# Kernel optimization log

Measured on AMD Instinct MI355X. Metric: run time of the kernel, lower is better.

## Reference

```python
import jax, jax.numpy as jnp
import numpy as np

Cin, E, L, M, H, Cout = 256, 16, 64, 64, 64, 256
B, N = 16, 2048
D = M + L * E  # hypernetwork input dim = 1088


def setup_inputs() -> dict:
    key = jax.random.key(0)
    ks = jax.random.split(key, 8)
    def lin(k, fan_in, shape):
        return jax.random.normal(k, shape, jnp.float32) / np.float32(np.sqrt(fan_in))
    return {
        "x0": jax.random.randint(ks[0], (B, N), 0, Cin),
        "emb": jax.random.normal(ks[1], (Cin, E), jnp.float32) * 0.02,
        "W_enc_w": lin(ks[2], D, (D, H)), "W_enc_b": jnp.zeros((H,), jnp.float32),
        "W_dec_w": lin(ks[3], H, (H, M * M)), "W_dec_b": jnp.zeros((M * M,), jnp.float32),
        "b_enc_w": lin(ks[4], D, (D, H)), "b_enc_b": jnp.zeros((H,), jnp.float32),
        "b_dec_w": lin(ks[5], H, (H, M)), "b_dec_b": jnp.zeros((M,), jnp.float32),
        "dec_w": lin(ks[6], M, (M, Cout)), "dec_b": jnp.zeros((Cout,), jnp.float32),
    }


def reference(x0, emb, W_enc_w, W_enc_b, W_dec_w, W_dec_b,
              b_enc_w, b_enc_b, b_dec_w, b_dec_b, dec_w, dec_b):
    Bq, Nq = x0.shape
    inv_ln2 = jnp.float32(1.0 / np.log(2.0))
    # left-pad with token id 0 (torch pad on int indices pads zeros -> embedding row 0)
    xp = jnp.concatenate([jnp.zeros((Bq, L), x0.dtype), x0], axis=-1)  # [B, N+L]
    e = emb[xp]  # [B, N+L, E]
    # window for step t = tokens t-L..t-1 of x0 = xp[:, t:t+L]
    idxs = jnp.arange(Nq)[:, None] + jnp.arange(L)[None, :]  # [N, L]
    win = e[:, idxs].reshape(Bq, Nq, L * E).transpose(1, 0, 2)  # [N, B, L*E]
    ys = x0.T  # [N, B]

    def mlp(x, ew, eb, dw, db):
        return jax.nn.sigmoid(x @ ew + eb) @ dw + db

    def step(m, xy):
        w, y = xy  # w: [B, L*E], y: [B]
        inp = jnp.concatenate([m, w], axis=-1)  # [B, M + L*E]
        Wm = mlp(inp, W_enc_w, W_enc_b, W_dec_w, W_dec_b).reshape(Bq, M, M)
        bm = mlp(inp, b_enc_w, b_enc_b, b_dec_w, b_dec_b)  # [B, M]
        m = jax.nn.sigmoid(jnp.einsum('bij,bj->bi', Wm, m) + bm)
        logits = m @ dec_w + dec_b  # [B, Cout]
        lse = jax.nn.log_softmax(logits)
        loss = -jnp.take_along_axis(lse, y[:, None], axis=1)[:, 0] * inv_ln2
        return m, loss

    m0 = jnp.zeros((Bq, M), jnp.float32)
    _, losses = jax.lax.scan(step, m0, (win, ys))  # losses: [N, B]
    return losses.reshape(-1)  # matches torch.cat(losses): time-major [N*B]
```

## Files before the change

### kernel.cpp

```cpp
#include <hip/hip_runtime.h>
#include <hip/hip_bf16.h>
#include <hip/hip_fp16.h>


typedef unsigned int uint_t;
typedef unsigned short us_t;
typedef unsigned long long u64_t;
typedef _Float16 h2_t __attribute__((ext_vector_type(2)));

#define POISON64 0xAAAAAAAAAAAAAAAAULL

__device__ __forceinline__ us_t f2bf(float f) {
    uint_t u = __float_as_uint(f);
    uint_t r = u + 0x7fffu + ((u >> 16) & 1u);
    return (us_t)(r >> 16);
}
__device__ __forceinline__ float bf2f(us_t s) {
    return __uint_as_float(((uint_t)s) << 16);
}
__device__ __forceinline__ float bflo(uint_t u) { return __uint_as_float(u << 16); }
__device__ __forceinline__ float bfhi(uint_t u) { return __uint_as_float(u & 0xffff0000u); }

__device__ __forceinline__ us_t f2h(float f) {
    __half h = __float2half(f);
    return *reinterpret_cast<us_t*>(&h);
}
__device__ __forceinline__ float h2f(us_t s) {
    __half h = *reinterpret_cast<__half*>(&s);
    return __half2float(h);
}
__device__ __forceinline__ h2_t u2h2(uint_t u) {
    union { uint_t u; h2_t h; } x; x.u = u; return x.h;
}

#if __has_builtin(__builtin_amdgcn_fdot2)
__device__ __forceinline__ float dot2f(uint_t a, uint_t b, float c) {
    return __builtin_amdgcn_fdot2(u2h2(a), u2h2(b), c, false);
}
#else
__device__ __forceinline__ float dot2f(uint_t a, uint_t b, float c) {
    h2_t x = u2h2(a), y = u2h2(b);
    return c + (float)x.x * (float)y.x + (float)x.y * (float)y.y;
}
#endif

#define DOT4(q, base, acc)                                              \
    acc = dot2f(q.x, mreg2u[(base) + 0], acc);                          \
    acc = dot2f(q.y, mreg2u[(base) + 1], acc);                          \
    acc = dot2f(q.z, mreg2u[(base) + 2], acc);                          \
    acc = dot2f(q.w, mreg2u[(base) + 3], acc);

__global__ void cvt_kernel(const float* __restrict__ Wdecw,
                           const float* __restrict__ decw,
                           const float* __restrict__ Wencw,
                           const float* __restrict__ bencw,
                           us_t* __restrict__ WdG, us_t* __restrict__ decwY,
                           us_t* __restrict__ EWmG) {
    int o = blockIdx.x * 256 + threadIdx.x;
    if (o < 262144) {
        int s = o >> 16;
        int idx = o & 65535;
        int k = idx & 7;
        int oo = (idx >> 3) & 1023;
        int jp = idx >> 13;
        int h = oo >> 4, il = oo & 15;
        int i = s * 16 + il;
        int j = jp * 8 + k;
        WdG[o] = f2h(Wdecw[h * 4096 + i * 64 + j]);
    } else if (o < 278528) {
        int oo = o - 262144;
        int k = oo & 3, lane = (oo >> 2) & 63, mm = oo >> 8;
        decwY[oo] = f2bf(decw[mm * 256 + k * 64 + lane]);
    } else if (o < 286720) {
        int oo = o - 278528;
        int kk = oo & 7, h2 = (oo >> 3) & 127, jp = oo >> 10;
        int j = jp * 8 + kk;
        float v = (h2 < 64) ? Wencw[j * 64 + h2] : bencw[j * 64 + (h2 - 64)];
        EWmG[oo] = f2h(v);
    }
}

__global__ void build_T(const float* __restrict__ emb, const float* __restrict__ Wencw,
                        const float* __restrict__ bencw, float* __restrict__ T) {
    int l = blockIdx.x >> 8, v = blockIdx.x & 255, h2 = threadIdx.x;
    float acc = 0.f;
#pragma unroll
    for (int e = 0; e < 16; ++e) {
        int d = 64 + l * 16 + e;
        float w = (h2 < 64) ? Wencw[d * 64 + h2] : bencw[d * 64 + (h2 - 64)];
        acc += emb[v * 16 + e] * w;
    }
    T[blockIdx.x * 128 + h2] = acc;
}

__global__ void build_P(const float* __restrict__ T, const int* __restrict__ x0,
                        const float* __restrict__ Wencb, const float* __restrict__ bencb,
                        float* __restrict__ P) {
    int t = blockIdx.x >> 4, b = blockIdx.x & 15, h2 = threadIdx.x;
    float acc = (h2 < 64) ? Wencb[h2] : bencb[h2 - 64];
    for (int l = 0; l < 64; ++l) {
        int p = t + l;
        int v = (p < 64) ? 0 : x0[b * 2048 + (p - 64)];
        acc += T[(l * 256 + v) * 128 + h2];
    }
    P[blockIdx.x * 128 + h2] = acc;
}

__global__ __launch_bounds__(512, 2) void recur(
    const float* __restrict__ bdecw, const float* __restrict__ bdecb,
    const float* __restrict__ Wdecb, const us_t* __restrict__ WdG,
    const us_t* __restrict__ EWmG, const float* __restrict__ P,
    u64_t* __restrict__ mhb) {
    const int b = blockIdx.x & 15, s = blockIdx.x >> 4;
    const int tid = threadIdx.x;

    extern __shared__ char smem[];
    us_t*   EWm2   = (us_t*)(smem + 131072);
    us_t*   wdbt_s = (us_t*)(smem + 147456);
    us_t*   bdec_s = (us_t*)(smem + 149632);
    float*  hw_s   = (float*)(smem + 151808);
    float*  hb_s   = (float*)(smem + 152064);
    float*  m_s    = (float*)(smem + 152320);
    float*  V_s    = (float*)(smem + 152576);
    float*  rp_s   = (float*)(smem + 156928);
    float*  bias_s = (float*)(smem + 157440);
    uint_t* m2_s   = (uint_t*)(smem + 157504);

    uint4 wreg[16];
    {
        const uint4* g4 = (const uint4*)WdG + s * 8192;
#pragma unroll
        for (int jp = 0; jp < 8; ++jp) {
            wreg[jp]     = g4[jp * 1024 + tid];
            wreg[8 + jp] = g4[jp * 1024 + tid + 512];
        }
    }
    {
        const uint4* g4 = (const uint4*)EWmG;
        uint4* l4 = (uint4*)EWm2;
        for (int k = tid; k < 1024; k += 512) l4[k] = g4[k];
    }
    for (int k = tid; k < 1024; k += 512) {
        int j = k >> 4, il = k & 15;
        wdbt_s[j * 17 + il] = f2bf(Wdecb[(s * 16 + il) * 64 + j]);
        bdec_s[j * 17 + il] = f2bf(bdecw[j * 64 + s * 16 + il]);
    }
    if (tid < 16) bias_s[tid] = bdecb[s * 16 + tid];
    if (tid < 64) m_s[tid] = 0.f;
    if (tid < 32) m2_s[tid] = 0u;
    __syncthreads();

    uint_t mreg2u[32];
#pragma unroll
    for (int j = 0; j < 32; ++j) mreg2u[j] = 0u;

    float preg = 0.f;
    if (tid < 128) preg = P[b * 128 + tid];

    const uint4* EW4 = (const uint4*)EWm2;
    const int hA = tid >> 4, ilA = tid & 15;

    for (int t = 0; t < 2048; ++t) {
        float pnext = 0.f;
        int tp = (t < 2047) ? (t + 1) : 2047;
        if (tid < 128) pnext = P[(tp * 16 + b) * 128 + tid];

        float a0 = 0.f, a1 = 0.f;
#pragma unroll
        for (int jp = 0; jp < 8; ++jp) {
            uint4 q0 = wreg[jp];
            uint4 q1 = wreg[8 + jp];
            DOT4(q0, jp * 4, a0);
            DOT4(q1, jp * 4, a1);
        }
        V_s[hA * 17 + ilA] = a0;
        V_s[(hA + 32) * 17 + ilA] = a1;

        if (tid < 128) {
            float acc = preg;
#pragma unroll
            for (int jp = 0; jp < 8; ++jp) {
                uint4 e = EW4[jp * 128 + tid];
                DOT4(e, jp * 4, acc);
            }
            float sg = 1.f / (1.f + __expf(-acc));
            if (tid < 64) hw_s[tid] = sg; else hb_s[tid - 64] = sg;
        }
        preg = pnext;
        __syncthreads();

        if (tid < 128) {
            int il = tid & 15, q = (tid >> 4) & 3;
            if (tid < 64) {
                float r = 0.f;
#pragma unroll
                for (int hh = 0; hh < 16; ++hh) {
                    int h = q * 16 + hh;
                    r += hw_s[h] * V_s[h * 17 + il];
                }
                rp_s[q * 16 + il] = r;
            } else {
                float r = 0.f;
#pragma unroll
                for (int kk = 0; kk < 16; ++kk) {
                    int jh = q * 16 + kk;
                    r += m_s[jh] * bf2f(wdbt_s[jh * 17 + il]);
                    r += hb_s[jh] * bf2f(bdec_s[jh * 17 + il]);
                }
                rp_s[64 + q * 16 + il] = r;
            }
        }
        __syncthreads();

        if (tid < 64) {
            u64_t* row = mhb + (u64_t)(t * 16 + b) * 16;
            float nmf = 0.f;
            if (tid < 16) {
                float r = bias_s[tid];
#pragma unroll
                for (int p = 0; p < 8; ++p) r += rp_s[p * 16 + tid];
                nmf = 1.f / (1.f + __expf(-r));
            }
            us_t nh = f2h(nmf);
            if (tid < 16) m_s[s * 16 + tid] = h2f(nh);
            uint_t nhu = (uint_t)nh;
            uint_t w0 = (uint_t)__shfl((int)nhu, (tid & 3) * 4 + 0, 64);
            uint_t w1 = (uint_t)__shfl((int)nhu, (tid & 3) * 4 + 1, 64);
            uint_t w2 = (uint_t)__shfl((int)nhu, (tid & 3) * 4 + 2, 64);
            uint_t w3 = (uint_t)__shfl((int)nhu, (tid & 3) * 4 + 3, 64);
            if (tid < 4) {
                u64_t pay = (u64_t)w0 | ((u64_t)w1 << 16)
                          | ((u64_t)w2 << 32) | ((u64_t)w3 << 48);
                __hip_atomic_store(row + s * 4 + tid, pay,
                                   __ATOMIC_RELAXED, __HIP_MEMORY_SCOPE_AGENT);
            }
            const bool self = (tid >> 2) == s;
            u64_t vk = 0;
            for (;;) {
                if (tid < 16 && !self)
                    vk = __hip_atomic_load(row + tid, __ATOMIC_RELAXED,
                                           __HIP_MEMORY_SCOPE_AGENT);
                bool ok = (tid >= 16) || self || (vk != POISON64);
                if (__ballot(ok) == ~0ull) break;
                __builtin_amdgcn_s_sleep(1);
            }
            if (tid < 16 && !self) {
                float4 mv;
                mv.x = h2f((us_t)(vk & 0xFFFFu));
                mv.y = h2f((us_t)((vk >> 16) & 0xFFFFu));
                mv.z = h2f((us_t)((vk >> 32) & 0xFFFFu));
                mv.w = h2f((us_t)(vk >> 48));
                ((float4*)m_s)[tid] = mv;
            }
            __builtin_amdgcn_s_waitcnt(0xC07F);
            if (tid < 32) {
                uint_t pk = (uint_t)f2h(m_s[2 * tid])
                          | ((uint_t)f2h(m_s[2 * tid + 1]) << 16);
                m2_s[tid] = pk;
            }
        }
        __syncthreads();

        {
            const uint4* mg = (const uint4*)m2_s;
#pragma unroll
            for (int p = 0; p < 8; ++p) {
                uint4 v = mg[p];
                mreg2u[p * 4 + 0] = v.x;
                mreg2u[p * 4 + 1] = v.y;
                mreg2u[p * 4 + 2] = v.z;
                mreg2u[p * 4 + 3] = v.w;
            }
        }
    }
}

__global__ __launch_bounds__(256) void loss_kernel(
    const us_t* __restrict__ mhb, const us_t* __restrict__ decwY,
    const float* __restrict__ decb, const int* __restrict__ x0,
    float* __restrict__ out) {
    __shared__ __align__(16) us_t dw[16384];
    const int tid = threadIdx.x;
    {
        const uint4* g4 = (const uint4*)decwY;
        uint4* l4 = (uint4*)dw;
        for (int k = tid; k < 2048; k += 256) l4[k] = g4[k];
    }
    __syncthreads();
    const int lane = tid & 63, wv = tid >> 6;
    const uint2* dwu2 = (const uint2*)dw;
    float b0 = decb[lane], b1 = decb[lane + 64];
    float b2 = decb[lane + 128], b3 = decb[lane + 192];
    for (int r = 0; r < 8; ++r) {
        int row = blockIdx.x * 32 + wv * 8 + r;
        float mL = h2f(mhb[row * 64 + lane]);
        float l0 = b0, l1 = b1, l2 = b2, l3 = b3;
#pragma unroll
        for (int mm = 0; mm < 64; ++mm) {
            float mv = __shfl(mL, mm, 64);
            uint2 q = dwu2[mm * 64 + lane];
            l0 += mv * bflo(q.x);
            l1 += mv * bfhi(q.x);
            l2 += mv * bflo(q.y);
            l3 += mv * bfhi(q.y);
        }
        float mx = fmaxf(fmaxf(l0, l1), fmaxf(l2, l3));
#pragma unroll
        for (int o = 32; o > 0; o >>= 1) mx = fmaxf(mx, __shfl_xor(mx, o, 64));
        float se = __expf(l0 - mx) + __expf(l1 - mx) + __expf(l2 - mx) + __expf(l3 - mx);
#pragma unroll
        for (int o = 32; o > 0; o >>= 1) se += __shfl_xor(se, o, 64);
        float lse = mx + __logf(se);
        int t = row >> 4, bb = row & 15;
        int y = x0[bb * 2048 + t];
        int hi = y >> 6;
        float cand = hi == 0 ? l0 : (hi == 1 ? l1 : (hi == 2 ? l2 : l3));
        float ly = __shfl(cand, y & 63, 64);
        if (lane == 0) out[row] = (lse - ly) * 1.4426950408889634f;
    }
}

extern "C" void kernel_launch(void* const* d_in, const int* in_sizes, int n_in,
                              void* d_out, int out_size, void* d_ws, size_t ws_size,
                              hipStream_t stream) {
    const int*   x0    = (const int*)d_in[0];
    const float* emb   = (const float*)d_in[1];
    const float* Wencw = (const float*)d_in[2];
    const float* Wencb = (const float*)d_in[3];
    const float* Wdecw = (const float*)d_in[4];
    const float* Wdecb = (const float*)d_in[5];
    const float* bencw = (const float*)d_in[6];
    const float* bencb = (const float*)d_in[7];
    const float* bdecw = (const float*)d_in[8];
    const float* bdecb = (const float*)d_in[9];
    const float* decw  = (const float*)d_in[10];
    const float* decb  = (const float*)d_in[11];
    float* out = (float*)d_out;

    char* ws = (char*)d_ws;
    us_t*  WdG   = (us_t*)(ws);
    us_t*  decwY = (us_t*)(ws + 524288);
    us_t*  EWmG  = (us_t*)(ws + 557056);
    float* T     = (float*)(ws + 573440);
    u64_t* mhb   = (u64_t*)T;
    float* P     = (float*)(ws + 8962048);

    static const int kRecurLds = 157632;
    (void)hipFuncSetAttribute((const void*)recur,
                              hipFuncAttributeMaxDynamicSharedMemorySize,
                              kRecurLds);

    cvt_kernel<<<1120, 256, 0, stream>>>(Wdecw, decw, Wencw, bencw,
                                         WdG, decwY, EWmG);
    build_T<<<16384, 128, 0, stream>>>(emb, Wencw, bencw, T);
    build_P<<<32768, 128, 0, stream>>>(T, x0, Wencb, bencb, P);
    (void)hipMemsetAsync(mhb, 0xAA, 4194304, stream);
    recur<<<64, 512, kRecurLds, stream>>>(bdecw, bdecb, Wdecb, WdG, EWmG,
                                          P, mhb);
    loss_kernel<<<1024, 256, 0, stream>>>((const us_t*)mhb, decwY, decb, x0, out);
}
```

Before: 3.964 ms.

## Split hypernetwork weight slice by hidden unit and exchange partial sums across blocks

```diff
diff --git a/kernel.cpp b/kernel.cpp
--- a/kernel.cpp
+++ b/kernel.cpp
@@ -8,15 +8,10 @@
 typedef unsigned long long u64_t;
 typedef _Float16 h2_t __attribute__((ext_vector_type(2)));
 
-#define POISON64 0xAAAAAAAAAAAAAAAAULL
-
 __device__ __forceinline__ us_t f2bf(float f) {
     uint_t u = __float_as_uint(f);
     uint_t r = u + 0x7fffu + ((u >> 16) & 1u);
     return (us_t)(r >> 16);
-}
-__device__ __forceinline__ float bf2f(us_t s) {
-    return __uint_as_float(((uint_t)s) << 16);
 }
 __device__ __forceinline__ float bflo(uint_t u) { return __uint_as_float(u << 16); }
 __device__ __forceinline__ float bfhi(uint_t u) { return __uint_as_float(u & 0xffff0000u); }
@@ -63,8 +58,8 @@
         int k = idx & 7;
         int oo = (idx >> 3) & 1023;
         int jp = idx >> 13;
-        int h = oo >> 4, il = oo & 15;
-        int i = s * 16 + il;
+        int h = s * 16 + (oo >> 6);
+        int i = oo & 63;
         int j = jp * 8 + k;
         WdG[o] = f2h(Wdecw[h * 4096 + i * 64 + j]);
     } else if (o < 278528) {
@@ -110,21 +105,22 @@
     const float* __restrict__ bdecw, const float* __restrict__ bdecb,
     const float* __restrict__ Wdecb, const us_t* __restrict__ WdG,
     const us_t* __restrict__ EWmG, const float* __restrict__ P,
-    u64_t* __restrict__ mhb) {
+    uint_t* __restrict__ mh32, u64_t* __restrict__ pxb) {
     const int b = blockIdx.x & 15, s = blockIdx.x >> 4;
     const int tid = threadIdx.x;
 
     extern __shared__ char smem[];
-    us_t*   EWm2   = (us_t*)(smem + 131072);
-    us_t*   wdbt_s = (us_t*)(smem + 147456);
-    us_t*   bdec_s = (us_t*)(smem + 149632);
-    float*  hw_s   = (float*)(smem + 151808);
-    float*  hb_s   = (float*)(smem + 152064);
-    float*  m_s    = (float*)(smem + 152320);
-    float*  V_s    = (float*)(smem + 152576);
-    float*  rp_s   = (float*)(smem + 156928);
-    float*  bias_s = (float*)(smem + 157440);
-    uint_t* m2_s   = (uint_t*)(smem + 157504);
+    us_t*   EWm2   = (us_t*)(smem);
+    uint_t* wdbt2  = (uint_t*)(smem + 16384);
+    uint_t* bdec2  = (uint_t*)(smem + 24576);
+    float*  V_s    = (float*)(smem + 32768);
+    float*  rp4_s  = (float*)(smem + 36928);
+    float*  wdbm2_s= (float*)(smem + 37952);
+    float*  hbb2_s = (float*)(smem + 38464);
+    float*  hw_s   = (float*)(smem + 38976);
+    uint_t* hb2_s  = (uint_t*)(smem + 39232);
+    uint_t* m2_s   = (uint_t*)(smem + 39360);
+    float*  bias_s = (float*)(smem + 39488);
 
     uint4 wreg[16];
     {
@@ -140,13 +136,14 @@
         uint4* l4 = (uint4*)EWm2;
         for (int k = tid; k < 1024; k += 512) l4[k] = g4[k];
     }
-    for (int k = tid; k < 1024; k += 512) {
-        int j = k >> 4, il = k & 15;
-        wdbt_s[j * 17 + il] = f2bf(Wdecb[(s * 16 + il) * 64 + j]);
-        bdec_s[j * 17 + il] = f2bf(bdecw[j * 64 + s * 16 + il]);
-    }
-    if (tid < 16) bias_s[tid] = bdecb[s * 16 + tid];
-    if (tid < 64) m_s[tid] = 0.f;
+    for (int k = tid; k < 2048; k += 512) {
+        int jj = k >> 6, i = k & 63;
+        wdbt2[k] = (uint_t)f2h(Wdecb[i * 64 + 2 * jj])
+                 | ((uint_t)f2h(Wdecb[i * 64 + 2 * jj + 1]) << 16);
+        bdec2[k] = (uint_t)f2h(bdecw[(2 * jj) * 64 + i])
+                 | ((uint_t)f2h(bdecw[(2 * jj + 1) * 64 + i]) << 16);
+    }
+    if (tid < 64) bias_s[tid] = bdecb[tid];
     if (tid < 32) m2_s[tid] = 0u;
     __syncthreads();
 
@@ -158,7 +155,8 @@
     if (tid < 128) preg = P[b * 128 + tid];
 
     const uint4* EW4 = (const uint4*)EWm2;
-    const int hA = tid >> 4, ilA = tid & 15;
+    const int hl = tid >> 6, iA = tid & 63;
+    const int w = tid >> 6;
 
     for (int t = 0; t < 2048; ++t) {
         float pnext = 0.f;
@@ -173,8 +171,8 @@
             DOT4(q0, jp * 4, a0);
             DOT4(q1, jp * 4, a1);
         }
-        V_s[hA * 17 + ilA] = a0;
-        V_s[(hA + 32) * 17 + ilA] = a1;
+        V_s[hl * 65 + iA] = a0;
+        V_s[(hl + 8) * 65 + iA] = a1;
 
         if (tid < 128) {
             float acc = preg;
@@ -184,79 +182,86 @@
                 DOT4(e, jp * 4, acc);
             }
             float sg = 1.f / (1.f + __expf(-acc));
-            if (tid < 64) hw_s[tid] = sg; else hb_s[tid - 64] = sg;
+            if (tid < 64) {
+                hw_s[tid] = sg;
+            } else {
+                int l = tid - 64;
+                float vlo = __shfl(sg, (l & 31) * 2, 64);
+                float vhi = __shfl(sg, (l & 31) * 2 + 1, 64);
+                if (l < 32)
+                    hb2_s[l] = (uint_t)f2h(vlo) | ((uint_t)f2h(vhi) << 16);
+            }
         }
         preg = pnext;
         __syncthreads();
 
-        if (tid < 128) {
-            int il = tid & 15, q = (tid >> 4) & 3;
-            if (tid < 64) {
-                float r = 0.f;
-#pragma unroll
-                for (int hh = 0; hh < 16; ++hh) {
-                    int h = q * 16 + hh;
-                    r += hw_s[h] * V_s[h * 17 + il];
+        u64_t* slotb = pxb + (u64_t)(((t & 1) * 16 + b) * 4) * 64;
+        const uint_t tg = (uint_t)(t + 1);
+
+        if (tid < 64) {
+            float r0 = 0.f, r1 = 0.f;
+#pragma unroll
+            for (int hh = 0; hh < 8; ++hh) {
+                r0 += hw_s[s * 16 + 2 * hh]     * V_s[(2 * hh) * 65 + tid];
+                r1 += hw_s[s * 16 + 2 * hh + 1] * V_s[(2 * hh + 1) * 65 + tid];
+            }
+            float rs = r0 + r1;
+            rp4_s[s * 64 + tid] = rs;
+            u64_t pay = ((u64_t)tg << 32) | (u64_t)__float_as_uint(rs);
+            __hip_atomic_store(slotb + s * 64 + tid, pay,
+                               __ATOMIC_RELAXED, __HIP_MEMORY_SCOPE_AGENT);
+        }
+
+        if (w < 3) {
+            int p = w + (w >= s ? 1 : 0);
+            int lane = tid & 63;
+            const u64_t* src = slotb + p * 64 + lane;
+            u64_t v;
+            for (;;) {
+                v = __hip_atomic_load(src, __ATOMIC_RELAXED,
+                                      __HIP_MEMORY_SCOPE_AGENT);
+                if (__ballot((uint_t)(v >> 32) == tg) == ~0ull) break;
+                __builtin_amdgcn_s_sleep(1);
+            }
+            rp4_s[p * 64 + lane] = __uint_as_float((uint_t)v);
+        } else if (w < 5) {
+            int i = tid & 63;
+            float wm = 0.f, hbv = 0.f;
+            if (w == 3) {
+#pragma unroll
+                for (int jj = 0; jj < 16; ++jj) {
+                    wm  = dot2f(wdbt2[jj * 64 + i], mreg2u[jj], wm);
+                    hbv = dot2f(bdec2[jj * 64 + i], hb2_s[jj], hbv);
                 }
-                rp_s[q * 16 + il] = r;
+                wdbm2_s[i] = wm;
+                hbb2_s[i] = hbv;
             } else {
-                float r = 0.f;
-#pragma unroll
-                for (int kk = 0; kk < 16; ++kk) {
-                    int jh = q * 16 + kk;
-                    r += m_s[jh] * bf2f(wdbt_s[jh * 17 + il]);
-                    r += hb_s[jh] * bf2f(bdec_s[jh * 17 + il]);
+#pragma unroll
+                for (int jj = 0; jj < 16; ++jj) {
+                    wm  = dot2f(wdbt2[(16 + jj) * 64 + i], mreg2u[16 + jj], wm);
+                    hbv = dot2f(bdec2[(16 + jj) * 64 + i], hb2_s[16 + jj], hbv);
                 }
-                rp_s[64 + q * 16 + il] = r;
+                wdbm2_s[64 + i] = wm;
+                hbb2_s[64 + i] = hbv;
             }
         }
         __syncthreads();
 
         if (tid < 64) {
-            u64_t* row = mhb + (u64_t)(t * 16 + b) * 16;
-            float nmf = 0.f;
-            if (tid < 16) {
-                float r = bias_s[tid];
-#pragma unroll
-                for (int p = 0; p < 8; ++p) r += rp_s[p * 16 + tid];
-                nmf = 1.f / (1.f + __expf(-r));
-            }
-            us_t nh = f2h(nmf);
-            if (tid < 16) m_s[s * 16 + tid] = h2f(nh);
+            float r = ((rp4_s[tid] + rp4_s[64 + tid])
+                     + (rp4_s[128 + tid] + rp4_s[192 + tid]))
+                    + (wdbm2_s[tid] + wdbm2_s[64 + tid])
+                    + (hbb2_s[tid] + hbb2_s[64 + tid])
+                    + bias_s[tid];
+            float nm = 1.f / (1.f + __expf(-r));
+            us_t nh = f2h(nm);
             uint_t nhu = (uint_t)nh;
-            uint_t w0 = (uint_t)__shfl((int)nhu, (tid & 3) * 4 + 0, 64);
-            uint_t w1 = (uint_t)__shfl((int)nhu, (tid & 3) * 4 + 1, 64);
-            uint_t w2 = (uint_t)__shfl((int)nhu, (tid & 3) * 4 + 2, 64);
-            uint_t w3 = (uint_t)__shfl((int)nhu, (tid & 3) * 4 + 3, 64);
-            if (tid < 4) {
-                u64_t pay = (u64_t)w0 | ((u64_t)w1 << 16)
-                          | ((u64_t)w2 << 32) | ((u64_t)w3 << 48);
-                __hip_atomic_store(row + s * 4 + tid, pay,
-                                   __ATOMIC_RELAXED, __HIP_MEMORY_SCOPE_AGENT);
-            }
-            const bool self = (tid >> 2) == s;
-            u64_t vk = 0;
-            for (;;) {
-                if (tid < 16 && !self)
-                    vk = __hip_atomic_load(row + tid, __ATOMIC_RELAXED,
-                                           __HIP_MEMORY_SCOPE_AGENT);
-                bool ok = (tid >= 16) || self || (vk != POISON64);
-                if (__ballot(ok) == ~0ull) break;
-                __builtin_amdgcn_s_sleep(1);
-            }
-            if (tid < 16 && !self) {
-                float4 mv;
-                mv.x = h2f((us_t)(vk & 0xFFFFu));
-                mv.y = h2f((us_t)((vk >> 16) & 0xFFFFu));
-                mv.z = h2f((us_t)((vk >> 32) & 0xFFFFu));
-                mv.w = h2f((us_t)(vk >> 48));
-                ((float4*)m_s)[tid] = mv;
-            }
-            __builtin_amdgcn_s_waitcnt(0xC07F);
+            uint_t lo = (uint_t)__shfl((int)nhu, (tid & 31) * 2, 64);
+            uint_t hi = (uint_t)__shfl((int)nhu, (tid & 31) * 2 + 1, 64);
             if (tid < 32) {
-                uint_t pk = (uint_t)f2h(m_s[2 * tid])
-                          | ((uint_t)f2h(m_s[2 * tid + 1]) << 16);
+                uint_t pk = lo | (hi << 16);
                 m2_s[tid] = pk;
+                if (s == 0) mh32[(t * 16 + b) * 32 + tid] = pk;
             }
         }
         __syncthreads();
@@ -338,12 +343,13 @@
     float* out = (float*)d_out;
 
     char* ws = (char*)d_ws;
-    us_t*  WdG   = (us_t*)(ws);
-    us_t*  decwY = (us_t*)(ws + 524288);
-    us_t*  EWmG  = (us_t*)(ws + 557056);
-    float* T     = (float*)(ws + 573440);
-    u64_t* mhb   = (u64_t*)T;
-    float* P     = (float*)(ws + 8962048);
+    us_t*   WdG   = (us_t*)(ws);
+    us_t*   decwY = (us_t*)(ws + 524288);
+    us_t*   EWmG  = (us_t*)(ws + 557056);
+    u64_t*  pxb   = (u64_t*)(ws + 573440);
+    float*  T     = (float*)(ws + 638976);
+    uint_t* mh32  = (uint_t*)T;
+    float*  P     = (float*)(ws + 9027584);
 
     static const int kRecurLds = 157632;
     (void)hipFuncSetAttribute((const void*)recur,
@@ -354,8 +360,8 @@
                                          WdG, decwY, EWmG);
     build_T<<<16384, 128, 0, stream>>>(emb, Wencw, bencw, T);
     build_P<<<32768, 128, 0, stream>>>(T, x0, Wencb, bencb, P);
-    (void)hipMemsetAsync(mhb, 0xAA, 4194304, stream);
+    (void)hipMemsetAsync(pxb, 0, 65536, stream);
     recur<<<64, 512, kRecurLds, stream>>>(bdecw, bdecb, Wdecb, WdG, EWmG,
-                                          P, mhb);
-    loss_kernel<<<1024, 256, 0, stream>>>((const us_t*)mhb, decwY, decb, x0, out);
-}
+                                          P, mh32, pxb);
+    loss_kernel<<<1024, 256, 0, stream>>>((const us_t*)mh32, decwY, decb, x0, out);
+}
```

Result: faster. 3.722 ms (-6.1%).
